# Kernel tuning notes

Measured on AMD Instinct MI355X. Metric: run time of the kernel, lower is better.

The kernel has to match this reference:

```python
import jax, jax.numpy as jnp
import numpy as np

BN_EPS = 1e-5


def gcn_conv(x, src, dst, n, W, b):
    # PyG GCNConv: h = x @ W; add self-loops; symmetric deg^{-1/2} norm; scatter-add; + bias
    h = x @ W
    sl = jnp.arange(n, dtype=src.dtype)
    src_f = jnp.concatenate([src, sl])
    dst_f = jnp.concatenate([dst, sl])
    deg = jax.ops.segment_sum(jnp.ones_like(dst_f, dtype=h.dtype), dst_f, num_segments=n)
    dis = jnp.where(deg > 0, jax.lax.rsqrt(jnp.maximum(deg, 1.0)), 0.0)
    norm = dis[src_f] * dis[dst_f]                       # [E+N]
    msg = h[src_f] * norm[:, None]                       # gather + scale
    out = jax.ops.segment_sum(msg, dst_f, num_segments=n)  # scatter-add
    return out + b


def batchnorm(x, g, b):
    # training-mode BatchNorm1d (batch statistics), deterministic
    mu = jnp.mean(x, axis=0)
    var = jnp.mean((x - mu) ** 2, axis=0)
    return g * (x - mu) * jax.lax.rsqrt(var + BN_EPS) + b


def setup_inputs() -> dict:
    key = jax.random.key(0)
    ks = jax.random.split(key, 12)
    N, E, F_IN, D, M, G = 40000, 640000, 128, 128, 256, 2000
    x = jax.random.normal(ks[0], (N, F_IN), dtype=jnp.float32)
    edge_index = jax.random.randint(ks[1], (2, E), 0, N, dtype=jnp.int64)
    batch = jnp.sort(jax.random.randint(ks[2], (N,), 0, G, dtype=jnp.int64))
    s = lambda fi: 1.0 / np.sqrt(fi)
    W1 = jax.random.normal(ks[3], (F_IN, D), dtype=jnp.float32) * s(F_IN)
    b1 = jnp.zeros((D,), jnp.float32)
    W2 = jax.random.normal(ks[4], (D, D), dtype=jnp.float32) * s(D)
    b2 = jnp.zeros((D,), jnp.float32)
    bn1_g = jnp.ones((D,), jnp.float32); bn1_b = jnp.zeros((D,), jnp.float32)
    bn2_g = jnp.ones((D,), jnp.float32); bn2_b = jnp.zeros((D,), jnp.float32)
    fc1_w = jax.random.normal(ks[5], (D, M), dtype=jnp.float32) * s(D)
    fc1_b = jnp.zeros((M,), jnp.float32)
    fc2_w = jax.random.normal(ks[6], (M, M), dtype=jnp.float32) * s(M)
    fc2_b = jnp.zeros((M,), jnp.float32)
    fc3_w = jax.random.normal(ks[7], (M, 1), dtype=jnp.float32) * s(M)
    fc3_b = jnp.zeros((1,), jnp.float32)
    return dict(x=x, edge_index=edge_index, batch=batch, num_graphs=G,
                W1=W1, b1=b1, W2=W2, b2=b2,
                bn1_g=bn1_g, bn1_b=bn1_b, bn2_g=bn2_g, bn2_b=bn2_b,
                fc1_w=fc1_w, fc1_b=fc1_b, fc2_w=fc2_w, fc2_b=fc2_b,
                fc3_w=fc3_w, fc3_b=fc3_b)


def reference(x, edge_index, batch, num_graphs, W1, b1, W2, b2,
              bn1_g, bn1_b, bn2_g, bn2_b,
              fc1_w, fc1_b, fc2_w, fc2_b, fc3_w, fc3_b):
    n = x.shape[0]
    src, dst = edge_index[0], edge_index[1]
    h = gcn_conv(x, src, dst, n, W1, b1)
    h = jax.nn.relu(batchnorm(h, bn1_g, bn1_b))
    h = gcn_conv(h, src, dst, n, W2, b2)
    h = jax.nn.relu(batchnorm(h, bn2_g, bn2_b))
    g = jax.ops.segment_sum(h, batch, num_segments=num_graphs)  # scatter_sum pooling [G, D]
    g = jax.nn.relu(g @ fc1_w + fc1_b)   # dropout is identity in eval
    g = jax.nn.relu(g @ fc2_w + fc2_b)
    return g @ fc3_w + fc3_b             # [G, 1]
```

## Files before the change

kernel.cpp:

```cpp
#include <hip/hip_runtime.h>
#include <hip/hip_fp16.h>

#define NN 40000
#define NE 640000
#define DF 128
#define NG 2000
#define NCH 157
#define FILLB 625
#define GT_BLKS 625
#define NCHUNK 16
#define ECH 40000
#define NOCT 8
#define QN 5120
#define NPAD (NOCT * QN)
#define NWIN 160
#define HISTB (NCHUNK * NOCT)

typedef unsigned int u32;
typedef __attribute__((ext_vector_type(8))) short short8;
typedef __attribute__((ext_vector_type(4))) float floatx4;

__device__ inline float2 bf2_to_f2(u32 u) {
    return make_float2(__uint_as_float(u << 16), __uint_as_float(u & 0xffff0000u));
}
__device__ inline u32 f_to_bf(float f) {
    u32 u = __float_as_uint(f);
    return (u + 0x7fffu + ((u >> 16) & 1u)) >> 16;
}
__device__ inline u32 pack_bf2(float a, float b) {
    return f_to_bf(a) | (f_to_bf(b) << 16);
}
__device__ inline float bf_to_f(short s) {
    return __uint_as_float(((u32)(unsigned short)s) << 16);
}
__device__ inline float colw_to_f(int cw) {
    return __half2float(__ushort_as_half((unsigned short)((u32)cw >> 16)));
}

template<bool BF16IN, bool FUSE_BN>
__device__ __forceinline__ void gemm_core(const void* __restrict__ Xv, const unsigned short* __restrict__ wt,
                                          u32* __restrict__ outb, const float* __restrict__ slots,
                                          const float* __restrict__ gam, const float* __restrict__ bet,
                                          int bid, char* sbuf, float* sc, float* sh) {
    unsigned short* wlds = (unsigned short*)sbuf;
    unsigned short* clds = (unsigned short*)sbuf;
    int tid = threadIdx.x;
    int row0 = bid * 64;

    if (FUSE_BN) {
        if (tid < 128) {
            float s = 0.f, q = 0.f;
            for (int k = 0; k < 64; k++) {
                s += slots[k * 256 + tid];
                q += slots[k * 256 + 128 + tid];
            }
            const float inv_n = 1.0f / (float)NN;
            float mu = s * inv_n;
            float va = fmaf(-mu, mu, q * inv_n);
            float a = gam[tid] * rsqrtf(va + 1e-5f);
            sc[tid] = a;
            sh[tid] = fmaf(-mu, a, bet[tid]);
        }
    }
    for (int i = tid; i < 2048; i += 256) {
        int c = i >> 4, s = i & 15;
        *(uint4*)&wlds[c * 128 + ((s ^ (c & 7)) << 3)] = ((const uint4*)wt)[i];
    }
    __syncthreads();

    int lane = tid & 63;
    int wave = tid >> 6;
    int qr = lane >> 4;
    int rl = lane & 15;

    int rA = row0 + wave * 16 + rl;
    floatx4 acc[8];
#pragma unroll
    for (int b = 0; b < 8; b++) acc[b] = (floatx4){0.f, 0.f, 0.f, 0.f};
#pragma unroll
    for (int kb = 0; kb < 4; kb++) {
        int k0 = kb * 32 + qr * 8;
        short8 a0;
        if (!BF16IN) {
            const float* p0 = (const float*)Xv + (size_t)rA * DF + k0;
            float4 u0 = *(const float4*)p0, u1 = *(const float4*)(p0 + 4);
            float fa[8] = {u0.x, u0.y, u0.z, u0.w, u1.x, u1.y, u1.z, u1.w};
#pragma unroll
            for (int j = 0; j < 8; j++) a0[j] = (short)f_to_bf(fa[j]);
        } else {
            a0 = *(const short8*)((const u32*)Xv + (size_t)rA * 64 + (k0 >> 1));
            if (FUSE_BN) {
#pragma unroll
                for (int j = 0; j < 8; j++) {
                    float f0 = fmaxf(fmaf(bf_to_f(a0[j]), sc[k0 + j], sh[k0 + j]), 0.f);
                    a0[j] = (short)f_to_bf(f0);
                }
            }
        }
#pragma unroll
        for (int ct = 0; ct < 8; ct++) {
            int rowB = ct * 16 + rl;
            short8 bfr = *(const short8*)&wlds[rowB * 128 + ((((kb << 2) + qr) ^ (rl & 7)) << 3)];
            acc[ct] = __builtin_amdgcn_mfma_f32_16x16x32_bf16(a0, bfr, acc[ct], 0, 0, 0);
        }
    }
    __syncthreads();
#pragma unroll
    for (int ct = 0; ct < 8; ct++)
#pragma unroll
        for (int r = 0; r < 4; r++) {
            int lr = wave * 16 + qr * 4 + r;
            int c = ct * 16 + rl;
            clds[lr * 128 + (((c >> 3) ^ (lr & 7)) << 3) + (c & 7)] = (unsigned short)f_to_bf(acc[ct][r]);
        }
    __syncthreads();
    for (int i = tid; i < 1024; i += 256) {
        int lr = i >> 4, s = i & 15;
        uint4 v = *(const uint4*)&clds[lr * 128 + ((s ^ (lr & 7)) << 3)];
        ((uint4*)(outb + (size_t)(row0 + lr) * 64))[s] = v;
    }
}

__global__ __launch_bounds__(256) void k_prep(const float* __restrict__ W1, const float* __restrict__ W2,
                                              unsigned short* __restrict__ wt1, unsigned short* __restrict__ wt2,
                                              float* __restrict__ slots0) {
    int bid = blockIdx.x, tid = threadIdx.x;
    if (bid < 64) {
        slots0[bid * 512 + tid] = 0.f;
        slots0[bid * 512 + 256 + tid] = 0.f;
    } else if (bid < 128) {
        int i = (bid - 64) * 256 + tid;
        wt1[i] = (unsigned short)f_to_bf(W1[(i & 127) * 128 + (i >> 7)]);
    } else {
        int i = (bid - 128) * 256 + tid;
        wt2[i] = (unsigned short)f_to_bf(W2[(i & 127) * 128 + (i >> 7)]);
    }
}

__global__ __launch_bounds__(256, 5) void k_countgemm(const int* __restrict__ dst,
                                                      int* __restrict__ degT, int* __restrict__ rank,
                                                      int* __restrict__ wsum,
                                                      const unsigned short* __restrict__ wt1,
                                                      const float* __restrict__ X, u32* __restrict__ outb) {
    __shared__ __align__(16) char sbuf[32768];
    int bid = blockIdx.x;
    int tid = threadIdx.x;
    if (bid < HISTB) {
        int c = bid >> 3, oct = bid & 7;
        int nlo = oct * QN;
        int* hist = (int*)sbuf;
        for (int i = tid; i < QN; i += 256) hist[i] = 0;
        __syncthreads();
        int ebase = c * ECH;
        const int4* dst4 = (const int4*)(dst + ebase);
        for (int i4 = tid; i4 < 10000; i4 += 256) {
            int4 d4 = dst4[i4];
            int e = ebase + i4 * 4;
            int t0 = d4.x - nlo, t1 = d4.y - nlo, t2 = d4.z - nlo, t3 = d4.w - nlo;
            if ((u32)t0 < (u32)QN) rank[e]     = atomicAdd(&hist[t0], 1);
            if ((u32)t1 < (u32)QN) rank[e + 1] = atomicAdd(&hist[t1], 1);
            if ((u32)t2 < (u32)QN) rank[e + 2] = atomicAdd(&hist[t2], 1);
            if ((u32)t3 < (u32)QN) rank[e + 3] = atomicAdd(&hist[t3], 1);
        }
        __syncthreads();
        for (int i = tid; i < QN; i += 256) degT[(size_t)c * NPAD + nlo + i] = hist[i];
        int wv = tid >> 6, lane = tid & 63;
        for (int lw = wv; lw < 20; lw += 4) {
            int v = hist[lw * 256 + lane] + hist[lw * 256 + 64 + lane]
                  + hist[lw * 256 + 128 + lane] + hist[lw * 256 + 192 + lane];
            for (int off = 32; off > 0; off >>= 1) v += __shfl_down(v, off);
            if (lane == 0) wsum[c * NWIN + oct * 20 + lw] = v;
        }
        return;
    }
    gemm_core<false, false>(X, wt1, outb, nullptr, nullptr, nullptr,
                            bid - HISTB, sbuf, nullptr, nullptr);
}

__global__ __launch_bounds__(256) void k_scan(const int* __restrict__ degT, const int* __restrict__ wsum,
                                              int* __restrict__ baseT,
                                              int* __restrict__ row_ptr, float* __restrict__ dis) {
    __shared__ int red[256];
    __shared__ int ls[256];
    int tid = threadIdx.x;
    int wnd = blockIdx.x;
    int part = 0;
    int wp = tid < NWIN ? tid : tid - NWIN;
    for (int idx = tid; idx < NCHUNK * NWIN; idx += 256) {
        if (wp < wnd) part += wsum[idx];
        wp += 96; if (wp >= NWIN) wp -= NWIN;
    }
    red[tid] = part;
    int n = wnd * 256 + tid;
    int run = 0;
#pragma unroll
    for (int c = 0; c < NCHUNK; c++) {
        int v = degT[(size_t)c * NPAD + n];
        baseT[(size_t)c * NPAD + n] = run;
        run += v;
    }
    int d = run;
    ls[tid] = d;
    __syncthreads();
#pragma unroll
    for (int off = 128; off > 0; off >>= 1) {
        if (tid < off) red[tid] += red[tid + off];
        __syncthreads();
    }
    int base = red[0];
#pragma unroll
    for (int off = 1; off < 256; off <<= 1) {
        int t = (tid >= off) ? ls[tid - off] : 0;
        __syncthreads();
        ls[tid] += t;
        __syncthreads();
    }
    if (n < NN) {
        int r = base + ls[tid] - d;
        row_ptr[n] = r;
        dis[n] = rsqrtf((float)(d + 1));
    }
    if (wnd == NCH - 1 && tid == 0) row_ptr[NN] = NE;
}

__global__ __launch_bounds__(256) void k_fill(const int* __restrict__ src, const int* __restrict__ dst,
                                              const int* __restrict__ rank, const int* __restrict__ row_ptr,
                                              const int* __restrict__ baseT,
                                              const float* __restrict__ dis, u32* __restrict__ col) {
    int i4 = blockIdx.x * 256 + threadIdx.x;
    int4 d4 = ((const int4*)dst)[i4];
    int4 s4 = ((const int4*)src)[i4];
    int4 r4 = ((const int4*)rank)[i4];
    int e = i4 * 4;
    int dd[4] = {d4.x, d4.y, d4.z, d4.w};
    int ss[4] = {s4.x, s4.y, s4.z, s4.w};
    int rr[4] = {r4.x, r4.y, r4.z, r4.w};
#pragma unroll
    for (int q = 0; q < 4; q++) {
        int c = (e + q) / ECH;
        u32 h = (u32)__half_as_ushort(__float2half(dis[ss[q]]));
        col[row_ptr[dd[q]] + baseT[(size_t)c * NPAD + dd[q]] + rr[q]] = (u32)ss[q] | (h << 16);
    }
}

__global__ __launch_bounds__(256, 4) void k_gemm2(const u32* __restrict__ Hb, const unsigned short* __restrict__ wt2,
                                                  u32* __restrict__ outb, const float* __restrict__ slots,
                                                  const float* __restrict__ gam, const float* __restrict__ bet) {
    __shared__ __align__(16) char sbuf[32768];
    __shared__ float sc[128], sh[128];
    gemm_core<true, true>(Hb, wt2, outb, slots, gam, bet, blockIdx.x, sbuf, sc, sh);
}

__global__ __launch_bounds__(256, 8) void k_gather(const u32* __restrict__ Hb, const int* __restrict__ row_ptr,
                                                   const u32* __restrict__ col, const float* __restrict__ dis,
                                                   const float* __restrict__ bias, u32* __restrict__ outb,
                                                   float* __restrict__ slots) {
    __shared__ float sred[4][128];
    __shared__ float qred[4][128];
    int t = threadIdx.x & 63;
    int wv = threadIdx.x >> 6;
    int node = blockIdx.x * 4 + wv;
    float di = dis[node];
    int lo = row_ptr[node], hi = row_ptr[node + 1];
    float2 acc;
    {
        float2 a = bf2_to_f2(Hb[(size_t)node * 64 + t]);
        acc = make_float2(a.x * di, a.y * di);
    }
    for (int base = lo; base < hi; base += 64) {
        int m = hi - base; if (m > 64) m = 64;
        int cw = 0;
        if (t < m) cw = (int)col[base + t];
        int ng = (m + 3) >> 2;
        int c[4]; u32 u[4];
#pragma unroll
        for (int q = 0; q < 4; q++) {
            int idx = q < m ? q : 0;
            c[q] = __shfl(cw, idx);
            u[q] = Hb[(size_t)(c[q] & 0xffff) * 64 + t];
        }
        for (int g = 1; g < ng; g++) {
            int c2[4]; u32 u2[4];
#pragma unroll
            for (int q = 0; q < 4; q++) {
                int ii = g * 4 + q;
                int idx = ii < m ? ii : 0;
                c2[q] = __shfl(cw, idx);
                u2[q] = Hb[(size_t)(c2[q] & 0xffff) * 64 + t];
            }
#pragma unroll
            for (int q = 0; q < 4; q++) {
                int ii = (g - 1) * 4 + q;
                float wq = ii < m ? colw_to_f(c[q]) : 0.f;
                float2 h = bf2_to_f2(u[q]);
                acc.x = fmaf(h.x, wq, acc.x);
                acc.y = fmaf(h.y, wq, acc.y);
            }
#pragma unroll
            for (int q = 0; q < 4; q++) { c[q] = c2[q]; u[q] = u2[q]; }
        }
#pragma unroll
        for (int q = 0; q < 4; q++) {
            int ii = (ng - 1) * 4 + q;
            float wq = ii < m ? colw_to_f(c[q]) : 0.f;
            float2 h = bf2_to_f2(u[q]);
            acc.x = fmaf(h.x, wq, acc.x);
            acc.y = fmaf(h.y, wq, acc.y);
        }
    }
    float2 b = ((const float2*)bias)[t];
    acc.x = fmaf(acc.x, di, b.x);
    acc.y = fmaf(acc.y, di, b.y);
    outb[(size_t)node * 64 + t] = pack_bf2(acc.x, acc.y);
    sred[wv][2 * t] = acc.x;     sred[wv][2 * t + 1] = acc.y;
    qred[wv][2 * t] = acc.x * acc.x; qred[wv][2 * t + 1] = acc.y * acc.y;
    __syncthreads();
    int tid = threadIdx.x;
    if (tid < 128) {
        float s = sred[0][tid] + sred[1][tid] + sred[2][tid] + sred[3][tid];
        float q = qred[0][tid] + qred[1][tid] + qred[2][tid] + qred[3][tid];
        int slot = blockIdx.x & 63;
        atomicAdd(&slots[slot * 256 + tid], s);
        atomicAdd(&slots[slot * 256 + 128 + tid], q);
    }
}

__global__ __launch_bounds__(256) void k_poolfc(const u32* __restrict__ Hb, const int* __restrict__ batch,
                                                const float* __restrict__ slots,
                                                const float* __restrict__ gam, const float* __restrict__ bet,
                                                const float* __restrict__ fc1w, const float* __restrict__ fc1b,
                                                const float* __restrict__ fc2w, const float* __restrict__ fc2b,
                                                const float* __restrict__ fc3w, const float* __restrict__ fc3b,
                                                float* __restrict__ out) {
    __shared__ float sc[128], sh[128];
    __shared__ float pooled[4][128];
    __shared__ float g1[4][256];
    __shared__ float g2[4][256];
    __shared__ int bnds[5];
    int tid = threadIdx.x;
    int gbase = blockIdx.x * 4;
    if (tid < 128) {
        float s = 0.f, q = 0.f;
        for (int k = 0; k < 64; k++) {
            s += slots[k * 256 + tid];
            q += slots[k * 256 + 128 + tid];
        }
        const float inv_n = 1.0f / (float)NN;
        float mu = s * inv_n;
        float va = fmaf(-mu, mu, q * inv_n);
        float a = gam[tid] * rsqrtf(va + 1e-5f);
        sc[tid] = a;
        sh[tid] = fmaf(-mu, a, bet[tid]);
    } else if (tid < 133) {
        int target = gbase + (tid - 128);
        int a = 0, b = NN;
        while (a < b) { int m = (a + b) >> 1; if (batch[m] < target) a = m + 1; else b = m; }
        bnds[tid - 128] = a;
    }
    __syncthreads();
    {
        int g = tid >> 6, p = tid & 63;
        int lo = bnds[g], hi = bnds[g + 1];
        float a0 = 0.f, a1 = 0.f;
        float sc0 = sc[2 * p], sh0 = sh[2 * p], sc1 = sc[2 * p + 1], sh1 = sh[2 * p + 1];
        for (int i = lo; i < hi; i++) {
            float2 v = bf2_to_f2(Hb[(size_t)i * 64 + p]);
            a0 += fmaxf(fmaf(v.x, sc0, sh0), 0.f);
            a1 += fmaxf(fmaf(v.y, sc1, sh1), 0.f);
        }
        pooled[g][2 * p] = a0;
        pooled[g][2 * p + 1] = a1;
    }
    __syncthreads();
    {
        float x0 = 0.f, x1 = 0.f, x2 = 0.f, x3 = 0.f;
        for (int k = 0; k < 128; k++) {
            float wv = fc1w[k * 256 + tid];
            x0 = fmaf(pooled[0][k], wv, x0);
            x1 = fmaf(pooled[1][k], wv, x1);
            x2 = fmaf(pooled[2][k], wv, x2);
            x3 = fmaf(pooled[3][k], wv, x3);
        }
        float bb = fc1b[tid];
        g1[0][tid] = fmaxf(x0 + bb, 0.f);
        g1[1][tid] = fmaxf(x1 + bb, 0.f);
        g1[2][tid] = fmaxf(x2 + bb, 0.f);
        g1[3][tid] = fmaxf(x3 + bb, 0.f);
    }
    __syncthreads();
    {
        float x0 = 0.f, x1 = 0.f, x2 = 0.f, x3 = 0.f;
        for (int k = 0; k < 256; k++) {
            float wv = fc2w[k * 256 + tid];
            x0 = fmaf(g1[0][k], wv, x0);
            x1 = fmaf(g1[1][k], wv, x1);
            x2 = fmaf(g1[2][k], wv, x2);
            x3 = fmaf(g1[3][k], wv, x3);
        }
        float bb = fc2b[tid];
        g2[0][tid] = fmaxf(x0 + bb, 0.f);
        g2[1][tid] = fmaxf(x1 + bb, 0.f);
        g2[2][tid] = fmaxf(x2 + bb, 0.f);
        g2[3][tid] = fmaxf(x3 + bb, 0.f);
    }
    __syncthreads();
    {
        int lane = tid & 63, wv = tid >> 6;
        float s = fmaf(g2[wv][lane], fc3w[lane],
                  fmaf(g2[wv][64 + lane], fc3w[64 + lane],
                  fmaf(g2[wv][128 + lane], fc3w[128 + lane],
                       g2[wv][192 + lane] * fc3w[192 + lane])));
        for (int off = 32; off > 0; off >>= 1) s += __shfl_down(s, off);
        if (lane == 0) out[gbase + wv] = s + fc3b[0];
    }
}

extern "C" void kernel_launch(void* const* d_in, const int* in_sizes, int n_in,
                              void* d_out, int out_size, void* d_ws, size_t ws_size,
                              hipStream_t stream) {
    const float* x    = (const float*)d_in[0];
    const int*   ei   = (const int*)d_in[1];
    const int*   batch= (const int*)d_in[2];
    const float* W1   = (const float*)d_in[4];
    const float* b1   = (const float*)d_in[5];
    const float* W2   = (const float*)d_in[6];
    const float* b2   = (const float*)d_in[7];
    const float* bn1g = (const float*)d_in[8];
    const float* bn1b = (const float*)d_in[9];
    const float* bn2g = (const float*)d_in[10];
    const float* bn2b = (const float*)d_in[11];
    const float* fc1w = (const float*)d_in[12];
    const float* fc1b = (const float*)d_in[13];
    const float* fc2w = (const float*)d_in[14];
    const float* fc2b = (const float*)d_in[15];
    const float* fc3w = (const float*)d_in[16];
    const float* fc3b = (const float*)d_in[17];
    const int* src = ei;
    const int* dst = ei + NE;
    float* outp = (float*)d_out;

    char* w = (char*)d_ws;
    size_t o = 0;
    auto alloc = [&](size_t bytes) -> char* {
        char* p = w + o;
        o = (o + bytes + 255) & ~(size_t)255;
        return p;
    };
    int*   degT    = (int*)alloc((size_t)NCHUNK * NPAD * 4);
    int*   baseT   = (int*)alloc((size_t)NCHUNK * NPAD * 4);
    int*   wsum    = (int*)alloc((size_t)NCHUNK * NWIN * 4);
    float* slots0  = (float*)alloc((size_t)2 * 64 * 256 * 4);
    int*   row_ptr = (int*)alloc((size_t)(NN + 1) * 4);
    int*   rank    = (int*)alloc((size_t)NE * 4);
    u32*   col     = (u32*)alloc((size_t)NE * 4);
    float* dis     = (float*)alloc((size_t)NN * 4);
    unsigned short* wt1 = (unsigned short*)alloc(128 * 128 * 2);
    unsigned short* wt2 = (unsigned short*)alloc(128 * 128 * 2);
    u32*   bufA    = (u32*)alloc((size_t)NN * 64 * 4);
    u32*   bufB    = (u32*)alloc((size_t)NN * 64 * 4);
    float* slotsA  = slots0;
    float* slotsB  = slots0 + 64 * 256;

    k_prep<<<192, 256, 0, stream>>>(W1, W2, wt1, wt2, slots0);
    k_countgemm<<<HISTB + GT_BLKS, 256, 0, stream>>>(dst, degT, rank, wsum, wt1, x, bufA);
    k_scan<<<NCH, 256, 0, stream>>>(degT, wsum, baseT, row_ptr, dis);
    k_fill<<<FILLB, 256, 0, stream>>>(src, dst, rank, row_ptr, baseT, dis, col);
    k_gather<<<NN / 4, 256, 0, stream>>>(bufA, row_ptr, col, dis, b1, bufB, slotsA);
    k_gemm2<<<GT_BLKS, 256, 0, stream>>>(bufB, wt2, bufA, slotsA, bn1g, bn1b);
    k_gather<<<NN / 4, 256, 0, stream>>>(bufA, row_ptr, col, dis, b2, bufB, slotsB);
    k_poolfc<<<NG / 4, 256, 0, stream>>>(bufB, batch, slotsB, bn2g, bn2b,
                                         fc1w, fc1b, fc2w, fc2b, fc3w, fc3b, outp);
}
```

Baseline: 245.6 us.

## Regroup prep, histogram, scan and first GEMM into two kernels; cut stat slots

The degree histogram moves into the weight-prep kernel, and the prefix scan is fused with the first feature GEMM. This removes one kernel launch and its inter-kernel gap while keeping the dependency order. The number of BatchNorm partial-sum slots drops from 64 to 16, which shrinks the reduction that readers perform but raises atomic contention per slot in the gather kernel.

```diff
diff --git a/kernel.cpp b/kernel.cpp
--- a/kernel.cpp
+++ b/kernel.cpp
@@ -15,6 +15,8 @@
 #define NPAD (NOCT * QN)
 #define NWIN 160
 #define HISTB (NCHUNK * NOCT)
+#define PREPB 144
+#define NSLOT 16
 
 typedef unsigned int u32;
 typedef __attribute__((ext_vector_type(8))) short short8;
@@ -50,7 +52,8 @@
     if (FUSE_BN) {
         if (tid < 128) {
             float s = 0.f, q = 0.f;
-            for (int k = 0; k < 64; k++) {
+#pragma unroll
+            for (int k = 0; k < NSLOT; k++) {
                 s += slots[k * 256 + tid];
                 q += slots[k * 256 + 128 + tid];
             }
@@ -121,106 +124,111 @@
     }
 }
 
-__global__ __launch_bounds__(256) void k_prep(const float* __restrict__ W1, const float* __restrict__ W2,
-                                              unsigned short* __restrict__ wt1, unsigned short* __restrict__ wt2,
-                                              float* __restrict__ slots0) {
+__global__ __launch_bounds__(256) void k_prephist(const float* __restrict__ W1, const float* __restrict__ W2,
+                                                  unsigned short* __restrict__ wt1, unsigned short* __restrict__ wt2,
+                                                  float* __restrict__ slots0,
+                                                  const int* __restrict__ dst,
+                                                  int* __restrict__ degT, int* __restrict__ rank,
+                                                  int* __restrict__ wsum) {
+    __shared__ __align__(16) char sbuf[20480];
     int bid = blockIdx.x, tid = threadIdx.x;
-    if (bid < 64) {
+    if (bid < 16) {
         slots0[bid * 512 + tid] = 0.f;
         slots0[bid * 512 + 256 + tid] = 0.f;
-    } else if (bid < 128) {
-        int i = (bid - 64) * 256 + tid;
+        return;
+    }
+    if (bid < 80) {
+        int i = (bid - 16) * 256 + tid;
         wt1[i] = (unsigned short)f_to_bf(W1[(i & 127) * 128 + (i >> 7)]);
-    } else {
-        int i = (bid - 128) * 256 + tid;
+        return;
+    }
+    if (bid < PREPB) {
+        int i = (bid - 80) * 256 + tid;
         wt2[i] = (unsigned short)f_to_bf(W2[(i & 127) * 128 + (i >> 7)]);
-    }
-}
-
-__global__ __launch_bounds__(256, 5) void k_countgemm(const int* __restrict__ dst,
-                                                      int* __restrict__ degT, int* __restrict__ rank,
-                                                      int* __restrict__ wsum,
-                                                      const unsigned short* __restrict__ wt1,
-                                                      const float* __restrict__ X, u32* __restrict__ outb) {
+        return;
+    }
+    int hb = bid - PREPB;
+    int c = hb >> 3, oct = hb & 7;
+    int nlo = oct * QN;
+    int* hist = (int*)sbuf;
+    for (int i = tid; i < QN; i += 256) hist[i] = 0;
+    __syncthreads();
+    int ebase = c * ECH;
+    const int4* dst4 = (const int4*)(dst + ebase);
+    for (int i4 = tid; i4 < 10000; i4 += 256) {
+        int4 d4 = dst4[i4];
+        int e = ebase + i4 * 4;
+        int t0 = d4.x - nlo, t1 = d4.y - nlo, t2 = d4.z - nlo, t3 = d4.w - nlo;
+        if ((u32)t0 < (u32)QN) rank[e]     = atomicAdd(&hist[t0], 1);
+        if ((u32)t1 < (u32)QN) rank[e + 1] = atomicAdd(&hist[t1], 1);
+        if ((u32)t2 < (u32)QN) rank[e + 2] = atomicAdd(&hist[t2], 1);
+        if ((u32)t3 < (u32)QN) rank[e + 3] = atomicAdd(&hist[t3], 1);
+    }
+    __syncthreads();
+    for (int i = tid; i < QN; i += 256) degT[(size_t)c * NPAD + nlo + i] = hist[i];
+    int wv = tid >> 6, lane = tid & 63;
+    for (int lw = wv; lw < 20; lw += 4) {
+        int v = hist[lw * 256 + lane] + hist[lw * 256 + 64 + lane]
+              + hist[lw * 256 + 128 + lane] + hist[lw * 256 + 192 + lane];
+        for (int off = 32; off > 0; off >>= 1) v += __shfl_down(v, off);
+        if (lane == 0) wsum[c * NWIN + oct * 20 + lw] = v;
+    }
+}
+
+__global__ __launch_bounds__(256, 5) void k_scangemm(const int* __restrict__ degT, const int* __restrict__ wsum,
+                                                     int* __restrict__ baseT,
+                                                     int* __restrict__ row_ptr, float* __restrict__ dis,
+                                                     const unsigned short* __restrict__ wt1,
+                                                     const float* __restrict__ X, u32* __restrict__ outb) {
     __shared__ __align__(16) char sbuf[32768];
+    int tid = threadIdx.x;
     int bid = blockIdx.x;
-    int tid = threadIdx.x;
-    if (bid < HISTB) {
-        int c = bid >> 3, oct = bid & 7;
-        int nlo = oct * QN;
-        int* hist = (int*)sbuf;
-        for (int i = tid; i < QN; i += 256) hist[i] = 0;
+    if (bid < NCH) {
+        int* red = (int*)sbuf;
+        int* ls  = (int*)(sbuf + 1024);
+        int wnd = bid;
+        int part = 0;
+        int wp = tid < NWIN ? tid : tid - NWIN;
+        for (int idx = tid; idx < NCHUNK * NWIN; idx += 256) {
+            if (wp < wnd) part += wsum[idx];
+            wp += 96; if (wp >= NWIN) wp -= NWIN;
+        }
+        red[tid] = part;
+        int n = wnd * 256 + tid;
+        int run = 0;
+#pragma unroll
+        for (int c = 0; c < NCHUNK; c++) {
+            int v = degT[(size_t)c * NPAD + n];
+            baseT[(size_t)c * NPAD + n] = run;
+            run += v;
+        }
+        int d = run;
+        ls[tid] = d;
         __syncthreads();
-        int ebase = c * ECH;
-        const int4* dst4 = (const int4*)(dst + ebase);
-        for (int i4 = tid; i4 < 10000; i4 += 256) {
-            int4 d4 = dst4[i4];
-            int e = ebase + i4 * 4;
-            int t0 = d4.x - nlo, t1 = d4.y - nlo, t2 = d4.z - nlo, t3 = d4.w - nlo;
-            if ((u32)t0 < (u32)QN) rank[e]     = atomicAdd(&hist[t0], 1);
-            if ((u32)t1 < (u32)QN) rank[e + 1] = atomicAdd(&hist[t1], 1);
-            if ((u32)t2 < (u32)QN) rank[e + 2] = atomicAdd(&hist[t2], 1);
-            if ((u32)t3 < (u32)QN) rank[e + 3] = atomicAdd(&hist[t3], 1);
-        }
-        __syncthreads();
-        for (int i = tid; i < QN; i += 256) degT[(size_t)c * NPAD + nlo + i] = hist[i];
-        int wv = tid >> 6, lane = tid & 63;
-        for (int lw = wv; lw < 20; lw += 4) {
-            int v = hist[lw * 256 + lane] + hist[lw * 256 + 64 + lane]
-                  + hist[lw * 256 + 128 + lane] + hist[lw * 256 + 192 + lane];
-            for (int off = 32; off > 0; off >>= 1) v += __shfl_down(v, off);
-            if (lane == 0) wsum[c * NWIN + oct * 20 + lw] = v;
-        }
+#pragma unroll
+        for (int off = 128; off > 0; off >>= 1) {
+            if (tid < off) red[tid] += red[tid + off];
+            __syncthreads();
+        }
+        int base = red[0];
+#pragma unroll
+        for (int off = 1; off < 256; off <<= 1) {
+            int t = (tid >= off) ? ls[tid - off] : 0;
+            __syncthreads();
+            ls[tid] += t;
+            __syncthreads();
+        }
+        if (n < NN) {
+            int r = base + ls[tid] - d;
+            row_ptr[n] = r;
+            dis[n] = rsqrtf((float)(d + 1));
+        }
+        if (wnd == NCH - 1 && tid == 0) row_ptr[NN] = NE;
         return;
     }
+    float* dummy = nullptr;
     gemm_core<false, false>(X, wt1, outb, nullptr, nullptr, nullptr,
-                            bid - HISTB, sbuf, nullptr, nullptr);
-}
-
-__global__ __launch_bounds__(256) void k_scan(const int* __restrict__ degT, const int* __restrict__ wsum,
-                                              int* __restrict__ baseT,
-                                              int* __restrict__ row_ptr, float* __restrict__ dis) {
-    __shared__ int red[256];
-    __shared__ int ls[256];
-    int tid = threadIdx.x;
-    int wnd = blockIdx.x;
-    int part = 0;
-    int wp = tid < NWIN ? tid : tid - NWIN;
-    for (int idx = tid; idx < NCHUNK * NWIN; idx += 256) {
-        if (wp < wnd) part += wsum[idx];
-        wp += 96; if (wp >= NWIN) wp -= NWIN;
-    }
-    red[tid] = part;
-    int n = wnd * 256 + tid;
-    int run = 0;
-#pragma unroll
-    for (int c = 0; c < NCHUNK; c++) {
-        int v = degT[(size_t)c * NPAD + n];
-        baseT[(size_t)c * NPAD + n] = run;
-        run += v;
-    }
-    int d = run;
-    ls[tid] = d;
-    __syncthreads();
-#pragma unroll
-    for (int off = 128; off > 0; off >>= 1) {
-        if (tid < off) red[tid] += red[tid + off];
-        __syncthreads();
-    }
-    int base = red[0];
-#pragma unroll
-    for (int off = 1; off < 256; off <<= 1) {
-        int t = (tid >= off) ? ls[tid - off] : 0;
-        __syncthreads();
-        ls[tid] += t;
-        __syncthreads();
-    }
-    if (n < NN) {
-        int r = base + ls[tid] - d;
-        row_ptr[n] = r;
-        dis[n] = rsqrtf((float)(d + 1));
-    }
-    if (wnd == NCH - 1 && tid == 0) row_ptr[NN] = NE;
+                            bid - NCH, sbuf, dummy, dummy);
 }
 
 __global__ __launch_bounds__(256) void k_fill(const int* __restrict__ src, const int* __restrict__ dst,
@@ -319,7 +327,7 @@
     if (tid < 128) {
         float s = sred[0][tid] + sred[1][tid] + sred[2][tid] + sred[3][tid];
         float q = qred[0][tid] + qred[1][tid] + qred[2][tid] + qred[3][tid];
-        int slot = blockIdx.x & 63;
+        int slot = blockIdx.x & (NSLOT - 1);
         atomicAdd(&slots[slot * 256 + tid], s);
         atomicAdd(&slots[slot * 256 + 128 + tid], q);
     }
@@ -341,7 +349,8 @@
     int gbase = blockIdx.x * 4;
     if (tid < 128) {
         float s = 0.f, q = 0.f;
-        for (int k = 0; k < 64; k++) {
+#pragma unroll
+        for (int k = 0; k < NSLOT; k++) {
             s += slots[k * 256 + tid];
             q += slots[k * 256 + 128 + tid];
         }
@@ -449,7 +458,7 @@
     int*   degT    = (int*)alloc((size_t)NCHUNK * NPAD * 4);
     int*   baseT   = (int*)alloc((size_t)NCHUNK * NPAD * 4);
     int*   wsum    = (int*)alloc((size_t)NCHUNK * NWIN * 4);
-    float* slots0  = (float*)alloc((size_t)2 * 64 * 256 * 4);
+    float* slots0  = (float*)alloc((size_t)2 * NSLOT * 256 * 4);
     int*   row_ptr = (int*)alloc((size_t)(NN + 1) * 4);
     int*   rank    = (int*)alloc((size_t)NE * 4);
     u32*   col     = (u32*)alloc((size_t)NE * 4);
@@ -459,11 +468,12 @@
     u32*   bufA    = (u32*)alloc((size_t)NN * 64 * 4);
     u32*   bufB    = (u32*)alloc((size_t)NN * 64 * 4);
     float* slotsA  = slots0;
-    float* slotsB  = slots0 + 64 * 256;
-
-    k_prep<<<192, 256, 0, stream>>>(W1, W2, wt1, wt2, slots0);
-    k_countgemm<<<HISTB + GT_BLKS, 256, 0, stream>>>(dst, degT, rank, wsum, wt1, x, bufA);
-    k_scan<<<NCH, 256, 0, stream>>>(degT, wsum, baseT, row_ptr, dis);
+    float* slotsB  = slots0 + NSLOT * 256;
+
+    k_prephist<<<PREPB + HISTB, 256, 0, stream>>>(W1, W2, wt1, wt2, slots0,
+                                                  dst, degT, rank, wsum);
+    k_scangemm<<<NCH + GT_BLKS, 256, 0, stream>>>(degT, wsum, baseT, row_ptr, dis,
+                                                  wt1, x, bufA);
     k_fill<<<FILLB, 256, 0, stream>>>(src, dst, rank, row_ptr, baseT, dis, col);
     k_gather<<<NN / 4, 256, 0, stream>>>(bufA, row_ptr, col, dis, b1, bufB, slotsA);
     k_gemm2<<<GT_BLKS, 256, 0, stream>>>(bufB, wt2, bufA, slotsA, bn1g, bn1b);
```

Measured after the change: 246.5 us. About the same (+0.4%).
